# Optimization experiments

Measured on AMD Instinct MI355X. Metric: run time of the kernel, lower is better.

## Reference

```python
import jax, jax.numpy as jnp
import numpy as np

B, T, S, E, H, A, DV = 32, 64, 64, 256, 512, 512, 32000
L = 2  # stacked LSTM layers


def setup_inputs() -> dict:
    key = jax.random.key(0)
    ks = jax.random.split(key, 16)
    g = lambda k, shape, s: jax.random.normal(k, shape, jnp.float32) * s
    return {
        "initial_input": g(ks[0], (B, T, E), 1.0),
        "hidden0": g(ks[1], (L, B, H), 1.0),
        "cell0": g(ks[2], (L, B, H), 1.0),
        "encoder_output": g(ks[3], (B, S, H), 1.0),
        "W1": g(ks[4], (H, A), 0.04),
        "b1": jnp.zeros((A,), jnp.float32),
        "W2": g(ks[5], (H, A), 0.04),
        "b2": jnp.zeros((A,), jnp.float32),
        "V": g(ks[6], (A,), 0.04),
        "bV": jnp.zeros((), jnp.float32),
        "Wx0": g(ks[7], (H + E, 4 * H), 0.03),
        "Wh0": g(ks[8], (H, 4 * H), 0.03),
        "bL0": jnp.zeros((4 * H,), jnp.float32),
        "Wx1": g(ks[9], (H, 4 * H), 0.03),
        "Wh1": g(ks[10], (H, 4 * H), 0.03),
        "bL1": jnp.zeros((4 * H,), jnp.float32),
        "Wd": g(ks[11], (H, DV), 0.03),
        "bd": jnp.zeros((DV,), jnp.float32),
        "seq_len": T,
    }


def _lstm_cell(x, h, c, Wx, Wh, b):
    # Keras LSTM cell math (inference: recurrent_dropout inactive).
    z = x @ Wx + h @ Wh + b  # [B, 4H]
    i, f, g, o = jnp.split(z, 4, axis=-1)
    i = jax.nn.sigmoid(i)
    f = jax.nn.sigmoid(f)
    o = jax.nn.sigmoid(o)
    c = f * c + i * jnp.tanh(g)
    h = o * jnp.tanh(c)
    return h, c


def reference(initial_input, hidden0, cell0, encoder_output,
              W1, b1, W2, b2, V, bV,
              Wx0, Wh0, bL0, Wx1, Wh1, bL1,
              Wd, bd, seq_len):
    # Precompute the encoder-side attention projection once (invariant over steps).
    enc_proj = encoder_output @ W2 + b2  # [B, S, A]

    def step(carry, x_t):
        h0, c0, h1, c1 = carry
        # Bahdanau attention: query = last layer's hidden state.
        q = h1 @ W1 + b1                               # [B, A]
        scores = jnp.tanh(enc_proj + q[:, None, :]) @ V + bV  # [B, S]
        attn = jax.nn.softmax(scores, axis=1)          # [B, S]
        context = jnp.einsum('bs,bsd->bd', attn, encoder_output)  # [B, H]
        # decoder input = concat(context, token embedding)
        x0 = jnp.concatenate([context, x_t], axis=-1)  # [B, H+E]
        h0, c0 = _lstm_cell(x0, h0, c0, Wx0, Wh0, bL0)
        h1, c1 = _lstm_cell(h0, h1, c1, Wx1, Wh1, bL1)
        logits = h1 @ Wd + bd                          # [B, DV]
        return (h0, c0, h1, c1), logits

    init = (hidden0[0], cell0[0], hidden0[1], cell0[1])
    xs = jnp.swapaxes(initial_input, 0, 1)  # [T, B, E]
    (h0, c0, h1, c1), outs = jax.lax.scan(step, init, xs)
    outputs = jnp.swapaxes(outs, 0, 1)      # [B, T, DV]
    hidden = jnp.stack([h0, h1])            # [L, B, H]
    cell = jnp.stack([c0, c1])              # [L, B, H]
    return outputs, hidden, cell
```

## Files before the change

### kernel.cpp

```cpp
#include <hip/hip_runtime.h>
#include <hip/hip_bf16.h>

#define B_  32
#define T_  64
#define S_  64
#define E_  256
#define H_  512
#define A_  512
#define DV_ 32000
#define H4_ 2048
#define NCAT_ 4608

typedef __attribute__((ext_vector_type(8))) short short8;
typedef __attribute__((ext_vector_type(4))) float floatx4;

__device__ __forceinline__ float fast_sigmoid(float x) {
    return 1.0f / (1.0f + __expf(-x));
}
__device__ __forceinline__ float fast_tanh(float x) {
    x = fminf(9.0f, fmaxf(-9.0f, x));
    float e = __expf(2.0f * x);
    return (e - 1.0f) / (e + 1.0f);
}
__device__ __forceinline__ unsigned short f2bf(float f) {
    union { float f; unsigned u; } v; v.f = f;
    unsigned r = (v.u + 0x7fffu + ((v.u >> 16) & 1u)) >> 16;
    return (unsigned short)r;
}

__global__ __launch_bounds__(256) void k_setup(
    const float* __restrict__ enc, const float* __restrict__ W2,
    const float* __restrict__ b2, const float* __restrict__ hidden0,
    const float* __restrict__ cell0,
    float* __restrict__ encp, float* __restrict__ h0buf,
    float* __restrict__ h1buf, float* __restrict__ c0, float* __restrict__ c1)
{
    int bid = blockIdx.x, tid = threadIdx.x;
    if (bid < 4096) {
        int eid = bid * 256 + tid;
        int r = eid >> 9;
        int n = eid & 511;
        const float* er = enc + (size_t)r * H_;
        float acc = b2[n];
#pragma unroll 4
        for (int k = 0; k < H_; ++k)
            acc = fmaf(er[k], W2[(size_t)k * A_ + n], acc);
        encp[(size_t)r * A_ + n] = acc;
    } else {
        int which = bid - 4096;
        const float* src = (which == 0) ? hidden0
                         : (which == 1) ? hidden0 + B_ * H_
                         : (which == 2) ? cell0
                         : cell0 + B_ * H_;
        float* dst = (which == 0) ? h0buf : (which == 1) ? h1buf
                   : (which == 2) ? c0 : c1;
        for (int i = tid; i < B_ * H_; i += 256) dst[i] = src[i];
    }
}

__global__ __launch_bounds__(256) void k_wdt(const float* __restrict__ Wd,
                                             unsigned short* __restrict__ WdT)
{
    __shared__ float tle[64 * 65];
    int kb = blockIdx.x & 7, nb = blockIdx.x >> 3;
    int k0 = kb * 64, n0 = nb * 64;
    int tid = threadIdx.x;
    for (int i = 0; i < 16; ++i) {
        int e = tid + 256 * i;
        int kk = e >> 6, nn = e & 63;
        tle[kk * 65 + nn] = Wd[(size_t)(k0 + kk) * DV_ + n0 + nn];
    }
    __syncthreads();
    for (int i = 0; i < 16; ++i) {
        int e = tid + 256 * i;
        int nn = e >> 6, kk = e & 63;
        WdT[(size_t)(n0 + nn) * H_ + k0 + kk] = f2bf(tle[kk * 65 + nn]);
    }
}

__global__ __launch_bounds__(256) void k_transpose(const float* __restrict__ src,
                                                   float* __restrict__ dst,
                                                   int K, int N)
{
    __shared__ float tle[64 * 65];
    int nt = N >> 6;
    int nb = blockIdx.x % nt, kb = blockIdx.x / nt;
    int k0 = kb * 64, n0 = nb * 64;
    int tid = threadIdx.x;
    for (int i = 0; i < 16; ++i) {
        int e = tid + 256 * i;
        int kk = e >> 6, nn = e & 63;
        tle[kk * 65 + nn] = src[(size_t)(k0 + kk) * N + n0 + nn];
    }
    __syncthreads();
    for (int i = 0; i < 16; ++i) {
        int e = tid + 256 * i;
        int nn = e >> 6, kk = e & 63;
        dst[(size_t)(n0 + nn) * K + k0 + kk] = tle[kk * 65 + nn];
    }
}

struct StepParams {
    const float *x, *enc;
    const float *b1, *V, *bV, *bL0, *bL1;
    const float *encp;
    const float *WcatT;
    const float *Wx0T;
    const float *Wx1T;
    float *qg, *p0g, *p1g, *ctx;
    float *h0buf, *h1buf, *c0, *c1;
    unsigned short *h1b;
    int t;
};

__global__ __launch_bounds__(256) void kA1(StepParams p)
{
    int bid = blockIdx.x, tid = threadIdx.x;
    int cur = p.t & 1;
    const float* h0c = p.h0buf + cur * (B_ * H_);
    const float* h1c = p.h1buf + cur * (B_ * H_);
    int b = tid >> 3, nl = tid & 7;
    int n = bid * 8 + nl;
    const float* src; float* dst; float bias;
    if (n < 512)       { src = h1c; dst = p.qg  + b * A_  + n;          bias = p.b1[n]; }
    else if (n < 2560) { src = h0c; dst = p.p0g + b * H4_ + (n - 512);  bias = 0.f; }
    else               { src = h1c; dst = p.p1g + b * H4_ + (n - 2560); bias = 0.f; }
    const float4* w4 = (const float4*)(p.WcatT + ((size_t)n << 9));
    const float4* h4 = (const float4*)(src + (b << 9));
    float ax = 0.f, ay = 0.f, az = 0.f, aw = 0.f;
#pragma unroll 8
    for (int kk = 0; kk < 128; ++kk) {
        float4 w = w4[kk], h = h4[kk];
        ax = fmaf(w.x, h.x, ax);
        ay = fmaf(w.y, h.y, ay);
        az = fmaf(w.z, h.z, az);
        aw = fmaf(w.w, h.w, aw);
    }
    *dst = (ax + ay) + (az + aw) + bias;
}

__global__ __launch_bounds__(256) void kA2(StepParams p)
{
    int b = blockIdx.x, tid = threadIdx.x;
    __shared__ float red2[256];
    __shared__ float qs[A_];
    __shared__ float smax[S_];
    qs[tid] = p.qg[b * A_ + tid];
    qs[tid + 256] = p.qg[b * A_ + tid + 256];
    __syncthreads();
    {
        int s = tid >> 2, pp = tid & 3;
        const float* ep = p.encp + ((size_t)(b * S_ + s)) * A_ + pp * 128;
        const float* qq = qs + pp * 128;
        const float* Vv = p.V + pp * 128;
        float acc = 0.f;
#pragma unroll 4
        for (int a = 0; a < 128; ++a)
            acc = fmaf(fast_tanh(ep[a] + qq[a]), Vv[a], acc);
        red2[tid] = acc;
    }
    __syncthreads();
    if (tid < 64) {
        float sv = red2[tid * 4] + red2[tid * 4 + 1] +
                   red2[tid * 4 + 2] + red2[tid * 4 + 3] + p.bV[0];
        float m = sv;
        for (int o = 32; o > 0; o >>= 1) m = fmaxf(m, __shfl_xor(m, o));
        float e = __expf(sv - m);
        float sum = e;
        for (int o = 32; o > 0; o >>= 1) sum += __shfl_xor(sum, o);
        smax[tid] = e / sum;
    }
    __syncthreads();
    {
        float a0 = 0.f, a1 = 0.f;
        for (int s2 = 0; s2 < S_; ++s2) {
            float at = smax[s2];
            const float* er = p.enc + ((size_t)(b * S_ + s2)) * H_;
            a0 = fmaf(at, er[tid], a0);
            a1 = fmaf(at, er[tid + 256], a1);
        }
        p.ctx[b * H_ + tid] = a0;
        p.ctx[b * H_ + tid + 256] = a1;
    }
}

__global__ __launch_bounds__(256) void kB(StepParams p)
{
    int bid = blockIdx.x, tid = threadIdx.x;
    int lane = tid & 63;
    int nxt = (p.t & 1) ^ 1;
    float* h0n = p.h0buf + nxt * (B_ * H_);
    int b = tid >> 3, jg = tid & 7;
    int j = bid * 2 + (jg & 1), g = jg >> 1;
    int n = j + (g << 9);
    const float4* w4 = (const float4*)(p.Wx0T + (size_t)n * 768);
    const float4* c4 = (const float4*)(p.ctx + (b << 9));
    const float4* x4 = (const float4*)(p.x + ((size_t)b * T_ + p.t) * E_);
    float ax = 0.f, ay = 0.f, az = 0.f, aw = 0.f;
#pragma unroll 8
    for (int kk = 0; kk < 128; ++kk) {
        float4 w = w4[kk], h = c4[kk];
        ax = fmaf(w.x, h.x, ax);
        ay = fmaf(w.y, h.y, ay);
        az = fmaf(w.z, h.z, az);
        aw = fmaf(w.w, h.w, aw);
    }
#pragma unroll 8
    for (int kk = 0; kk < 64; ++kk) {
        float4 w = w4[128 + kk], h = x4[kk];
        ax = fmaf(w.x, h.x, ax);
        ay = fmaf(w.y, h.y, ay);
        az = fmaf(w.z, h.z, az);
        aw = fmaf(w.w, h.w, aw);
    }
    float acc = p.p0g[b * H4_ + n] + p.bL0[n] + (ax + ay) + (az + aw);
    int lb = lane & ~7, jj = jg & 1;
    float z_f = __shfl(acc, lb + jj + 2);
    float z_g = __shfl(acc, lb + jj + 4);
    float z_o = __shfl(acc, lb + jj + 6);
    if (jg < 2) {
        float ii = fast_sigmoid(acc);
        float ff = fast_sigmoid(z_f);
        float gg = fast_tanh(z_g);
        float oo = fast_sigmoid(z_o);
        float cn = ff * p.c0[b * H_ + j] + ii * gg;
        float hn = oo * fast_tanh(cn);
        p.c0[b * H_ + j] = cn;
        h0n[b * H_ + j] = hn;
    }
}

__global__ __launch_bounds__(256) void kC(StepParams p)
{
    int bid = blockIdx.x, tid = threadIdx.x;
    int lane = tid & 63;
    int nxt = (p.t & 1) ^ 1;
    const float* h0n = p.h0buf + nxt * (B_ * H_);
    float*       h1n = p.h1buf + nxt * (B_ * H_);
    int b = tid >> 3, jg = tid & 7;
    int j = bid * 2 + (jg & 1), g = jg >> 1;
    int n = j + (g << 9);
    const float4* w4 = (const float4*)(p.Wx1T + ((size_t)n << 9));
    const float4* h4 = (const float4*)(h0n + (b << 9));
    float ax = 0.f, ay = 0.f, az = 0.f, aw = 0.f;
#pragma unroll 8
    for (int kk = 0; kk < 128; ++kk) {
        float4 w = w4[kk], h = h4[kk];
        ax = fmaf(w.x, h.x, ax);
        ay = fmaf(w.y, h.y, ay);
        az = fmaf(w.z, h.z, az);
        aw = fmaf(w.w, h.w, aw);
    }
    float acc = p.p1g[b * H4_ + n] + p.bL1[n] + (ax + ay) + (az + aw);
    int lb = lane & ~7, jj = jg & 1;
    float z_f = __shfl(acc, lb + jj + 2);
    float z_g = __shfl(acc, lb + jj + 4);
    float z_o = __shfl(acc, lb + jj + 6);
    if (jg < 2) {
        float ii = fast_sigmoid(acc);
        float ff = fast_sigmoid(z_f);
        float gg = fast_tanh(z_g);
        float oo = fast_sigmoid(z_o);
        float cn = ff * p.c1[b * H_ + j] + ii * gg;
        float hn = oo * fast_tanh(cn);
        p.c1[b * H_ + j] = cn;
        h1n[b * H_ + j] = hn;
        p.h1b[((size_t)p.t * B_ + b) * H_ + j] = f2bf(hn);
    }
}

__global__ __launch_bounds__(256) void k_tail(
    const float* __restrict__ h0buf, const float* __restrict__ h1buf,
    const float* __restrict__ c0, const float* __restrict__ c1,
    float* __restrict__ out_hc)
{
    int idx = blockIdx.x * 256 + threadIdx.x;
    out_hc[idx]               = h0buf[idx];
    out_hc[B_ * H_ + idx]     = h1buf[idx];
    out_hc[2 * B_ * H_ + idx] = c0[idx];
    out_hc[3 * B_ * H_ + idx] = c1[idx];
}

__global__ __launch_bounds__(256) void k_logits(
    const unsigned short* __restrict__ Am,
    const unsigned short* __restrict__ Bm,
    const float* __restrict__ bd,
    float* __restrict__ out)
{
    __shared__ __align__(16) unsigned short As[128 * 72];
    __shared__ __align__(16) unsigned short Bs[128 * 72];
    int tid = threadIdx.x;
    int lane = tid & 63, wv = tid >> 6;
    int mt = blockIdx.x & 15, nt = blockIdx.x >> 4;
    int m0 = mt * 128, n0 = nt * 128;
    int wm = wv >> 1, wn = wv & 1;

    floatx4 acc[4][4];
    for (int i = 0; i < 4; ++i)
        for (int j = 0; j < 4; ++j)
            acc[i][j] = (floatx4){0.f, 0.f, 0.f, 0.f};

    for (int kt = 0; kt < 8; ++kt) {
        int k0 = kt * 64;
        __syncthreads();
        for (int i = 0; i < 4; ++i) {
            int chunk = tid + 256 * i;
            int row = chunk >> 3, c8 = chunk & 7;
            uint4 va = *(const uint4*)(Am + (size_t)(m0 + row) * H_ + k0 + c8 * 8);
            *(uint4*)(As + row * 72 + c8 * 8) = va;
            uint4 vb = *(const uint4*)(Bm + (size_t)(n0 + row) * H_ + k0 + c8 * 8);
            *(uint4*)(Bs + row * 72 + c8 * 8) = vb;
        }
        __syncthreads();
        int q8 = (lane >> 4) * 8;
        int rl = lane & 15;
        for (int kk = 0; kk < 64; kk += 32) {
            short8 af[4], bf[4];
            for (int mi = 0; mi < 4; ++mi)
                af[mi] = *(const short8*)(As + (wm * 64 + mi * 16 + rl) * 72 + kk + q8);
            for (int ni = 0; ni < 4; ++ni)
                bf[ni] = *(const short8*)(Bs + (wn * 64 + ni * 16 + rl) * 72 + kk + q8);
            for (int mi = 0; mi < 4; ++mi)
                for (int ni = 0; ni < 4; ++ni)
                    acc[mi][ni] = __builtin_amdgcn_mfma_f32_16x16x32_bf16(
                        af[mi], bf[ni], acc[mi][ni], 0, 0, 0);
        }
    }

    int rl = lane & 15, qd = lane >> 4;
    for (int ni = 0; ni < 4; ++ni) {
        int n = n0 + wn * 64 + ni * 16 + rl;
        float bias = bd[n];
        for (int mi = 0; mi < 4; ++mi) {
            for (int r = 0; r < 4; ++r) {
                int m = m0 + wm * 64 + mi * 16 + qd * 4 + r;
                int tt = m >> 5, bb = m & 31;
                out[((size_t)(bb * T_ + tt)) * DV_ + n] = acc[mi][ni][r] + bias;
            }
        }
    }
}

extern "C" void kernel_launch(void* const* d_in, const int* in_sizes, int n_in,
                              void* d_out, int out_size, void* d_ws, size_t ws_size,
                              hipStream_t stream)
{
    const float* x       = (const float*)d_in[0];
    const float* hidden0 = (const float*)d_in[1];
    const float* cell0   = (const float*)d_in[2];
    const float* enc     = (const float*)d_in[3];
    const float* W1      = (const float*)d_in[4];
    const float* b1      = (const float*)d_in[5];
    const float* W2      = (const float*)d_in[6];
    const float* b2      = (const float*)d_in[7];
    const float* V       = (const float*)d_in[8];
    const float* bV      = (const float*)d_in[9];
    const float* Wx0     = (const float*)d_in[10];
    const float* Wh0     = (const float*)d_in[11];
    const float* bL0     = (const float*)d_in[12];
    const float* Wx1     = (const float*)d_in[13];
    const float* Wh1     = (const float*)d_in[14];
    const float* bL1     = (const float*)d_in[15];
    const float* Wd      = (const float*)d_in[16];
    const float* bd      = (const float*)d_in[17];

    char* ws = (char*)d_ws;
    size_t off = 0;
    auto alloc = [&](size_t bytes) -> void* {
        void* ptr = ws + off;
        off = (off + bytes + 255) & ~(size_t)255;
        return ptr;
    };
    unsigned short* WdT = (unsigned short*)alloc((size_t)DV_ * H_ * 2);
    float* encp  = (float*)alloc((size_t)B_ * S_ * A_ * 4);
    float* qg    = (float*)alloc((size_t)B_ * A_ * 4);
    float* p0g   = (float*)alloc((size_t)B_ * H4_ * 4);
    float* p1g   = (float*)alloc((size_t)B_ * H4_ * 4);
    float* ctx   = (float*)alloc((size_t)B_ * H_ * 4);
    float* h0buf = (float*)alloc((size_t)2 * B_ * H_ * 4);
    float* h1buf = (float*)alloc((size_t)2 * B_ * H_ * 4);
    float* c0    = (float*)alloc((size_t)B_ * H_ * 4);
    float* c1    = (float*)alloc((size_t)B_ * H_ * 4);
    unsigned short* h1b = (unsigned short*)alloc((size_t)T_ * B_ * H_ * 2);

    char* sc = (char*)d_out;
    size_t soff = 0;
    auto salloc = [&](size_t bytes) -> void* {
        void* ptr = sc + soff;
        soff = (soff + bytes + 255) & ~(size_t)255;
        return ptr;
    };
    float* WcatT = (float*)salloc((size_t)NCAT_ * H_ * 4);
    float* Wx0T  = (float*)salloc((size_t)H4_ * 768 * 4);
    float* Wx1T  = (float*)salloc((size_t)H4_ * H_ * 4);

    float* out = (float*)d_out;
    float* out_hc = out + (size_t)B_ * T_ * DV_;

    hipLaunchKernelGGL(k_setup, dim3(4100), dim3(256), 0, stream,
                       enc, W2, b2, hidden0, cell0, encp, h0buf, h1buf, c0, c1);
    hipLaunchKernelGGL(k_wdt, dim3(4000), dim3(256), 0, stream, Wd, WdT);
    hipLaunchKernelGGL(k_transpose, dim3(64),  dim3(256), 0, stream, W1,  WcatT,              512, 512);
    hipLaunchKernelGGL(k_transpose, dim3(256), dim3(256), 0, stream, Wh0, WcatT + 512 * 512,  512, 2048);
    hipLaunchKernelGGL(k_transpose, dim3(256), dim3(256), 0, stream, Wh1, WcatT + 2560 * 512, 512, 2048);
    hipLaunchKernelGGL(k_transpose, dim3(384), dim3(256), 0, stream, Wx0, Wx0T,               768, 2048);
    hipLaunchKernelGGL(k_transpose, dim3(256), dim3(256), 0, stream, Wx1, Wx1T,               512, 2048);

    StepParams sp;
    sp.x = x; sp.enc = enc;
    sp.b1 = b1; sp.V = V; sp.bV = bV; sp.bL0 = bL0; sp.bL1 = bL1;
    sp.encp = encp;
    sp.WcatT = WcatT; sp.Wx0T = Wx0T; sp.Wx1T = Wx1T;
    sp.qg = qg; sp.p0g = p0g; sp.p1g = p1g; sp.ctx = ctx;
    sp.h0buf = h0buf; sp.h1buf = h1buf; sp.c0 = c0; sp.c1 = c1;
    sp.h1b = h1b;

    for (int t = 0; t < T_; ++t) {
        sp.t = t;
        hipLaunchKernelGGL(kA1, dim3(576), dim3(256), 0, stream, sp);
        hipLaunchKernelGGL(kA2, dim3(32),  dim3(256), 0, stream, sp);
        hipLaunchKernelGGL(kB,  dim3(256), dim3(256), 0, stream, sp);
        hipLaunchKernelGGL(kC,  dim3(256), dim3(256), 0, stream, sp);
    }
    hipLaunchKernelGGL(k_tail, dim3(64), dim3(256), 0, stream,
                       h0buf, h1buf, c0, c1, out_hc);

    hipLaunchKernelGGL(k_logits, dim3(4000), dim3(256), 0, stream, h1b, WdT, bd, out);
}
```

Before: 8.402 ms.

## Precompute encoder·Wx0 and input projections to fuse context and LSTM0 into attention kernel

```diff
diff --git a/kernel.cpp b/kernel.cpp
--- a/kernel.cpp
+++ b/kernel.cpp
@@ -100,14 +100,94 @@
     }
 }
 
+__global__ __launch_bounds__(256) void k_encwx0(const float* __restrict__ enc,
+                                                const float* __restrict__ Wx0,
+                                                float* __restrict__ out)
+{
+    __shared__ float er[8][H_];
+    int blk = blockIdx.x;
+    int b = blk >> 3, st = blk & 7;
+    int tid = threadIdx.x;
+    for (int i = tid; i < 8 * H_; i += 256) {
+        int si = i >> 9, k = i & 511;
+        er[si][k] = enc[((size_t)(b * S_ + st * 8 + si)) * H_ + k];
+    }
+    __syncthreads();
+    float acc[8][8];
+#pragma unroll
+    for (int si = 0; si < 8; ++si)
+#pragma unroll
+        for (int i = 0; i < 8; ++i) acc[si][i] = 0.f;
+    for (int k = 0; k < H_; ++k) {
+        const float* wr = Wx0 + (size_t)k * H4_ + tid;
+        float w[8];
+#pragma unroll
+        for (int i = 0; i < 8; ++i) w[i] = wr[i * 256];
+#pragma unroll
+        for (int si = 0; si < 8; ++si) {
+            float e = er[si][k];
+#pragma unroll
+            for (int i = 0; i < 8; ++i)
+                acc[si][i] = fmaf(e, w[i], acc[si][i]);
+        }
+    }
+    for (int si = 0; si < 8; ++si) {
+        float* o = out + ((size_t)(b * S_ + st * 8 + si)) * H4_ + tid;
+#pragma unroll
+        for (int i = 0; i < 8; ++i) o[i * 256] = acc[si][i];
+    }
+}
+
+__global__ __launch_bounds__(256) void k_xproj(const float* __restrict__ x,
+                                               const float* __restrict__ Wx0,
+                                               const float* __restrict__ bL0,
+                                               float* __restrict__ xproj)
+{
+    __shared__ float xr[8][E_];
+    int blk = blockIdx.x;
+    int b = blk >> 3, tt = blk & 7;
+    int tid = threadIdx.x;
+    for (int i = tid; i < 8 * E_; i += 256) {
+        int ti = i >> 8, k = i & 255;
+        xr[ti][k] = x[((size_t)b * T_ + tt * 8 + ti) * E_ + k];
+    }
+    __syncthreads();
+    float bl[8];
+#pragma unroll
+    for (int i = 0; i < 8; ++i) bl[i] = bL0[tid + i * 256];
+    float acc[8][8];
+#pragma unroll
+    for (int si = 0; si < 8; ++si)
+#pragma unroll
+        for (int i = 0; i < 8; ++i) acc[si][i] = bl[i];
+    for (int k = 0; k < E_; ++k) {
+        const float* wr = Wx0 + (size_t)(H_ + k) * H4_ + tid;
+        float w[8];
+#pragma unroll
+        for (int i = 0; i < 8; ++i) w[i] = wr[i * 256];
+#pragma unroll
+        for (int si = 0; si < 8; ++si) {
+            float e = xr[si][k];
+#pragma unroll
+            for (int i = 0; i < 8; ++i)
+                acc[si][i] = fmaf(e, w[i], acc[si][i]);
+        }
+    }
+    for (int si = 0; si < 8; ++si) {
+        float* o = xproj + ((size_t)b * T_ + tt * 8 + si) * H4_ + tid;
+#pragma unroll
+        for (int i = 0; i < 8; ++i) o[i * 256] = acc[si][i];
+    }
+}
+
 struct StepParams {
-    const float *x, *enc;
-    const float *b1, *V, *bV, *bL0, *bL1;
+    const float *b1, *V, *bV, *bL1;
     const float *encp;
     const float *WcatT;
-    const float *Wx0T;
     const float *Wx1T;
-    float *qg, *p0g, *p1g, *ctx;
+    const float *encWx0;
+    const float *xproj;
+    float *qg, *p0g, *p1g;
     float *h0buf, *h1buf, *c0, *c1;
     unsigned short *h1b;
     int t;
@@ -139,7 +219,7 @@
     *dst = (ax + ay) + (az + aw) + bias;
 }
 
-__global__ __launch_bounds__(256) void kA2(StepParams p)
+__global__ __launch_bounds__(256) void kA2B(StepParams p)
 {
     int b = blockIdx.x, tid = threadIdx.x;
     __shared__ float red2[256];
@@ -171,58 +251,34 @@
         smax[tid] = e / sum;
     }
     __syncthreads();
-    {
-        float a0 = 0.f, a1 = 0.f;
-        for (int s2 = 0; s2 < S_; ++s2) {
-            float at = smax[s2];
-            const float* er = p.enc + ((size_t)(b * S_ + s2)) * H_;
-            a0 = fmaf(at, er[tid], a0);
-            a1 = fmaf(at, er[tid + 256], a1);
-        }
-        p.ctx[b * H_ + tid] = a0;
-        p.ctx[b * H_ + tid + 256] = a1;
-    }
-}
-
-__global__ __launch_bounds__(256) void kB(StepParams p)
-{
-    int bid = blockIdx.x, tid = threadIdx.x;
-    int lane = tid & 63;
+
+    float acc8[8];
+#pragma unroll
+    for (int i = 0; i < 8; ++i) acc8[i] = 0.f;
+    const float* ew = p.encWx0 + (size_t)b * (S_ * H4_);
+    for (int s = 0; s < S_; ++s) {
+        float a = smax[s];
+        const float* er = ew + (size_t)s * H4_ + tid;
+#pragma unroll
+        for (int i = 0; i < 8; ++i)
+            acc8[i] = fmaf(a, er[i * 256], acc8[i]);
+    }
+
+    const float* p0r = p.p0g + b * H4_;
+    const float* xpr = p.xproj + ((size_t)b * T_ + p.t) * H4_;
     int nxt = (p.t & 1) ^ 1;
     float* h0n = p.h0buf + nxt * (B_ * H_);
-    int b = tid >> 3, jg = tid & 7;
-    int j = bid * 2 + (jg & 1), g = jg >> 1;
-    int n = j + (g << 9);
-    const float4* w4 = (const float4*)(p.Wx0T + (size_t)n * 768);
-    const float4* c4 = (const float4*)(p.ctx + (b << 9));
-    const float4* x4 = (const float4*)(p.x + ((size_t)b * T_ + p.t) * E_);
-    float ax = 0.f, ay = 0.f, az = 0.f, aw = 0.f;
-#pragma unroll 8
-    for (int kk = 0; kk < 128; ++kk) {
-        float4 w = w4[kk], h = c4[kk];
-        ax = fmaf(w.x, h.x, ax);
-        ay = fmaf(w.y, h.y, ay);
-        az = fmaf(w.z, h.z, az);
-        aw = fmaf(w.w, h.w, aw);
-    }
-#pragma unroll 8
-    for (int kk = 0; kk < 64; ++kk) {
-        float4 w = w4[128 + kk], h = x4[kk];
-        ax = fmaf(w.x, h.x, ax);
-        ay = fmaf(w.y, h.y, ay);
-        az = fmaf(w.z, h.z, az);
-        aw = fmaf(w.w, h.w, aw);
-    }
-    float acc = p.p0g[b * H4_ + n] + p.bL0[n] + (ax + ay) + (az + aw);
-    int lb = lane & ~7, jj = jg & 1;
-    float z_f = __shfl(acc, lb + jj + 2);
-    float z_g = __shfl(acc, lb + jj + 4);
-    float z_o = __shfl(acc, lb + jj + 6);
-    if (jg < 2) {
-        float ii = fast_sigmoid(acc);
-        float ff = fast_sigmoid(z_f);
-        float gg = fast_tanh(z_g);
-        float oo = fast_sigmoid(z_o);
+#pragma unroll
+    for (int half = 0; half < 2; ++half) {
+        int j = tid + half * 256;
+        float zi = acc8[half + 0] + p0r[j]        + xpr[j];
+        float zf = acc8[half + 2] + p0r[j + 512]  + xpr[j + 512];
+        float zg = acc8[half + 4] + p0r[j + 1024] + xpr[j + 1024];
+        float zo = acc8[half + 6] + p0r[j + 1536] + xpr[j + 1536];
+        float ii = fast_sigmoid(zi);
+        float ff = fast_sigmoid(zf);
+        float gg = fast_tanh(zg);
+        float oo = fast_sigmoid(zo);
         float cn = ff * p.c0[b * H_ + j] + ii * gg;
         float hn = oo * fast_tanh(cn);
         p.c0[b * H_ + j] = cn;
@@ -376,7 +432,7 @@
     float* qg    = (float*)alloc((size_t)B_ * A_ * 4);
     float* p0g   = (float*)alloc((size_t)B_ * H4_ * 4);
     float* p1g   = (float*)alloc((size_t)B_ * H4_ * 4);
-    float* ctx   = (float*)alloc((size_t)B_ * H_ * 4);
+    float* ctx   = (float*)alloc((size_t)B_ * H_ * 4);   (void)ctx;
     float* h0buf = (float*)alloc((size_t)2 * B_ * H_ * 4);
     float* h1buf = (float*)alloc((size_t)2 * B_ * H_ * 4);
     float* c0    = (float*)alloc((size_t)B_ * H_ * 4);
@@ -390,9 +446,10 @@
         soff = (soff + bytes + 255) & ~(size_t)255;
         return ptr;
     };
-    float* WcatT = (float*)salloc((size_t)NCAT_ * H_ * 4);
-    float* Wx0T  = (float*)salloc((size_t)H4_ * 768 * 4);
-    float* Wx1T  = (float*)salloc((size_t)H4_ * H_ * 4);
+    float* WcatT  = (float*)salloc((size_t)NCAT_ * H_ * 4);
+    float* Wx1T   = (float*)salloc((size_t)H4_ * H_ * 4);
+    float* encWx0 = (float*)salloc((size_t)B_ * S_ * H4_ * 4);
+    float* xproj  = (float*)salloc((size_t)B_ * T_ * H4_ * 4);
 
     float* out = (float*)d_out;
     float* out_hc = out + (size_t)B_ * T_ * DV_;
@@ -403,24 +460,24 @@
     hipLaunchKernelGGL(k_transpose, dim3(64),  dim3(256), 0, stream, W1,  WcatT,              512, 512);
     hipLaunchKernelGGL(k_transpose, dim3(256), dim3(256), 0, stream, Wh0, WcatT + 512 * 512,  512, 2048);
     hipLaunchKernelGGL(k_transpose, dim3(256), dim3(256), 0, stream, Wh1, WcatT + 2560 * 512, 512, 2048);
-    hipLaunchKernelGGL(k_transpose, dim3(384), dim3(256), 0, stream, Wx0, Wx0T,               768, 2048);
     hipLaunchKernelGGL(k_transpose, dim3(256), dim3(256), 0, stream, Wx1, Wx1T,               512, 2048);
+    hipLaunchKernelGGL(k_encwx0, dim3(256), dim3(256), 0, stream, enc, Wx0, encWx0);
+    hipLaunchKernelGGL(k_xproj,  dim3(256), dim3(256), 0, stream, x, Wx0, bL0, xproj);
 
     StepParams sp;
-    sp.x = x; sp.enc = enc;
-    sp.b1 = b1; sp.V = V; sp.bV = bV; sp.bL0 = bL0; sp.bL1 = bL1;
+    sp.b1 = b1; sp.V = V; sp.bV = bV; sp.bL1 = bL1;
     sp.encp = encp;
-    sp.WcatT = WcatT; sp.Wx0T = Wx0T; sp.Wx1T = Wx1T;
-    sp.qg = qg; sp.p0g = p0g; sp.p1g = p1g; sp.ctx = ctx;
+    sp.WcatT = WcatT; sp.Wx1T = Wx1T;
+    sp.encWx0 = encWx0; sp.xproj = xproj;
+    sp.qg = qg; sp.p0g = p0g; sp.p1g = p1g;
     sp.h0buf = h0buf; sp.h1buf = h1buf; sp.c0 = c0; sp.c1 = c1;
     sp.h1b = h1b;
 
     for (int t = 0; t < T_; ++t) {
         sp.t = t;
-        hipLaunchKernelGGL(kA1, dim3(576), dim3(256), 0, stream, sp);
-        hipLaunchKernelGGL(kA2, dim3(32),  dim3(256), 0, stream, sp);
-        hipLaunchKernelGGL(kB,  dim3(256), dim3(256), 0, stream, sp);
-        hipLaunchKernelGGL(kC,  dim3(256), dim3(256), 0, stream, sp);
+        hipLaunchKernelGGL(kA1,  dim3(576), dim3(256), 0, stream, sp);
+        hipLaunchKernelGGL(kA2B, dim3(32),  dim3(256), 0, stream, sp);
+        hipLaunchKernelGGL(kC,   dim3(256), dim3(256), 0, stream, sp);
     }
     hipLaunchKernelGGL(k_tail, dim3(64), dim3(256), 0, stream,
                        h0buf, h1buf, c0, c1, out_hc);
```

New measurement: 7.112 ms. 1.18x faster.
